# Optimization experiments

Measured on AMD Instinct MI355X. Metric: run time of the kernel, lower is better.

The kernel has to match this reference:

```python
import jax, jax.numpy as jnp
import numpy as np

V, S, D, H, F, L, C = 30522, 1024, 1024, 16, 4096, 3, 5
HD = D // H
EPS = 1e-5


def layer_norm(x, g, b):
    mu = jnp.mean(x, axis=-1, keepdims=True)
    var = jnp.mean((x - mu) ** 2, axis=-1, keepdims=True)
    return (x - mu) * jax.lax.rsqrt(var + EPS) * g + b


def setup_inputs() -> dict:
    key = jax.random.key(0)
    ks = iter(jax.random.split(key, 32))
    s = 0.02
    inp = {
        "input_ids": jax.random.randint(next(ks), (8, S), 0, V),
        "attention_mask": jax.random.randint(next(ks), (8, S), 0, 2),
        "emb": jax.random.normal(next(ks), (V, D), jnp.float32) * s,
        "pos_emb": jax.random.normal(next(ks), (1, S, D), jnp.float32) * s,
        "Wq": jax.random.normal(next(ks), (L, D, D), jnp.float32) * s,
        "bq": jnp.zeros((L, D), jnp.float32),
        "Wk": jax.random.normal(next(ks), (L, D, D), jnp.float32) * s,
        "bk": jnp.zeros((L, D), jnp.float32),
        "Wv": jax.random.normal(next(ks), (L, D, D), jnp.float32) * s,
        "bv": jnp.zeros((L, D), jnp.float32),
        "Wo": jax.random.normal(next(ks), (L, D, D), jnp.float32) * s,
        "bo": jnp.zeros((L, D), jnp.float32),
        "ln1_g": jnp.ones((L, D), jnp.float32),
        "ln1_b": jnp.zeros((L, D), jnp.float32),
        "ln2_g": jnp.ones((L, D), jnp.float32),
        "ln2_b": jnp.zeros((L, D), jnp.float32),
        "W1": jax.random.normal(next(ks), (L, D, F), jnp.float32) * s,
        "b1": jnp.zeros((L, F), jnp.float32),
        "W2": jax.random.normal(next(ks), (L, F, D), jnp.float32) * s,
        "b2": jnp.zeros((L, D), jnp.float32),
        "cls_g": jnp.ones((D,), jnp.float32),
        "cls_b": jnp.zeros((D,), jnp.float32),
        "Wc": jax.random.normal(next(ks), (D, C), jnp.float32) * s,
        "bc": jnp.zeros((C,), jnp.float32),
    }
    return inp


def reference(input_ids, attention_mask, emb, pos_emb, Wq, bq, Wk, bk, Wv, bv,
              Wo, bo, ln1_g, ln1_b, ln2_g, ln2_b, W1, b1, W2, b2,
              cls_g, cls_b, Wc, bc):
    B, Sq = input_ids.shape
    x = emb[input_ids] + pos_emb[:, :Sq, :]  # [B,S,D]
    # mask: [B,1,1,S] broadcast over query positions
    mask = (attention_mask == 0)[:, None, None, :]
    for l in range(L):
        q = (x @ Wq[l] + bq[l]).reshape(B, Sq, H, HD).transpose(0, 2, 1, 3)
        k = (x @ Wk[l] + bk[l]).reshape(B, Sq, H, HD).transpose(0, 2, 1, 3)
        v = (x @ Wv[l] + bv[l]).reshape(B, Sq, H, HD).transpose(0, 2, 1, 3)
        scores = jnp.einsum('bhqd,bhkd->bhqk', q, k) / (HD ** 0.5)
        scores = jnp.where(mask, -1e9, scores)
        attn = jax.nn.softmax(scores, axis=-1)
        ctx = jnp.einsum('bhqk,bhkd->bhqd', attn, v)
        ctx = ctx.transpose(0, 2, 1, 3).reshape(B, Sq, D)
        attn_out = ctx @ Wo[l] + bo[l]
        x = layer_norm(x + attn_out, ln1_g[l], ln1_b[l])
        ff = jax.nn.gelu(x @ W1[l] + b1[l], approximate=False) @ W2[l] + b2[l]
        x = layer_norm(x + ff, ln2_g[l], ln2_b[l])
    cls_tok = x[:, 0, :]
    logits = layer_norm(cls_tok, cls_g, cls_b) @ Wc + bc
    return logits
```

## Files before the change

kernel.cpp:

```cpp
#include <hip/hip_runtime.h>
#include <math.h>

constexpr int S  = 1024;
constexpr int D  = 1024;
constexpr int H  = 16;
constexpr int F  = 4096;
constexpr int NL = 3;
constexpr int C  = 5;
constexpr int HD = 64;
constexpr int B  = 8;
constexpr int MTOK = B * S;

typedef unsigned short u16;
typedef __attribute__((ext_vector_type(4))) float f32x4;
typedef __attribute__((ext_vector_type(4))) int   i32x4;

__device__ inline u16 f2b(float x) {
  unsigned u = __float_as_uint(x);
  unsigned r = (u + 0x7fffu + ((u >> 16) & 1u)) >> 16;
  return (u16)r;
}
__device__ inline float b2f(u16 b) {
  return __uint_as_float(((unsigned)b) << 16);
}

#define GLD16(gptr, lptr)                                                  \
  __builtin_amdgcn_global_load_lds(                                        \
      (const __attribute__((address_space(1))) void*)(gptr),               \
      (__attribute__((address_space(3))) void*)(lptr), 16, 0, 0)

__device__ inline void mfma16(f32x4& acc, i32x4 a, i32x4 b) {
  asm("v_mfma_f32_16x16x32_bf16 %0, %1, %2, %0" : "+v"(acc) : "v"(a), "v"(b));
}

__device__ inline float block_reduce_sum_256(float v, float* red) {
  #pragma unroll
  for (int off = 32; off > 0; off >>= 1) v += __shfl_down(v, off, 64);
  int lane = threadIdx.x & 63, wid = threadIdx.x >> 6;
  if (lane == 0) red[wid] = v;
  __syncthreads();
  float t = red[0] + red[1] + red[2] + red[3];
  __syncthreads();
  return t;
}

__device__ inline float gelu_f(float x) {
  return 0.5f * x * (1.0f + erff(x * 0.70710678118654752f));
}

__global__ __launch_bounds__(256) void embed_kernel(
    const int* __restrict__ ids, const float* __restrict__ emb,
    const float* __restrict__ pos, float* __restrict__ X,
    u16* __restrict__ Xb) {
  int t = blockIdx.x;
  int s = t & (S - 1);
  size_t id = (size_t)ids[t];
  const float4* e = (const float4*)(emb + id * (size_t)D);
  const float4* p = (const float4*)(pos + (size_t)s * D);
  int i = threadIdx.x;
  float4 a = e[i], b = p[i];
  float4 v = make_float4(a.x + b.x, a.y + b.y, a.z + b.z, a.w + b.w);
  ((float4*)(X + (size_t)t * D))[i] = v;
  ushort4 o = {f2b(v.x), f2b(v.y), f2b(v.z), f2b(v.w)};
  *(ushort4*)&Xb[(size_t)t * D + i * 4] = o;
}

__global__ __launch_bounds__(256) void add_ln_kernel(
    const float* __restrict__ X, const float* __restrict__ Y,
    const float* __restrict__ g, const float* __restrict__ bta,
    float* __restrict__ Out, u16* __restrict__ Outb) {
  __shared__ float red[4];
  int t = blockIdx.x, i = threadIdx.x;
  const float4* xr = (const float4*)(X + (size_t)t * D);
  const float4* yr = (const float4*)(Y + (size_t)t * D);
  float4 a = xr[i], b = yr[i];
  float4 v = make_float4(a.x + b.x, a.y + b.y, a.z + b.z, a.w + b.w);
  float sum = v.x + v.y + v.z + v.w;
  sum = block_reduce_sum_256(sum, red);
  float mean = sum * (1.0f / D);
  float dx = v.x - mean, dy = v.y - mean, dz = v.z - mean, dw = v.w - mean;
  float sq = dx * dx + dy * dy + dz * dz + dw * dw;
  sq = block_reduce_sum_256(sq, red);
  float rstd = rsqrtf(sq * (1.0f / D) + 1e-5f);
  float4 gg = ((const float4*)g)[i];
  float4 bb = ((const float4*)bta)[i];
  float4 o = make_float4(dx * rstd * gg.x + bb.x, dy * rstd * gg.y + bb.y,
                         dz * rstd * gg.z + bb.z, dw * rstd * gg.w + bb.w);
  ((float4*)(Out + (size_t)t * D))[i] = o;
  ushort4 ob = {f2b(o.x), f2b(o.y), f2b(o.z), f2b(o.w)};
  *(ushort4*)&Outb[(size_t)t * D + i * 4] = ob;
}

__global__ __launch_bounds__(256) void transpose_cast_kernel(
    const float* __restrict__ W, u16* __restrict__ WT, int K, int N) {
  __shared__ float t[32][33];
  int r = threadIdx.x >> 3, c4 = (threadIdx.x & 7) * 4;
  *(float4*)&t[r][c4] =
      *(const float4*)&W[(size_t)(blockIdx.y * 32 + r) * N + blockIdx.x * 32 + c4];
  __syncthreads();
  int n = blockIdx.x * 32 + r;
  int k = blockIdx.y * 32 + c4;
  ushort4 o = {f2b(t[c4 + 0][r]), f2b(t[c4 + 1][r]),
               f2b(t[c4 + 2][r]), f2b(t[c4 + 3][r])};
  *(ushort4*)&WT[(size_t)n * K + k] = o;
}

template <int MODE>
__global__ __launch_bounds__(256) void gemm_mfma(
    const u16* __restrict__ A, const u16* __restrict__ BT,
    const float* __restrict__ bias, void* __restrict__ Cout,
    int M, int N, int K) {
  __shared__ u16 As[128][32];
  __shared__ u16 Bs[128][32];
  int tid = threadIdx.x;
  int row0 = blockIdx.y * 128, col0 = blockIdx.x * 128;
  int wid = tid >> 6, lane = tid & 63;
  int wr = (wid >> 1) * 64, wc = (wid & 1) * 64;
  int fr = lane & 15, fq = lane >> 4;

  f32x4 acc[4][4];
  #pragma unroll
  for (int m = 0; m < 4; m++)
    #pragma unroll
    for (int n = 0; n < 4; n++) acc[m][n] = (f32x4)(0.0f);

  for (int kt = 0; kt < K; kt += 32) {
    #pragma unroll
    for (int i = 0; i < 2; i++) {
      int f = i * 256 + tid;
      int r = f >> 2, ks = (f & 3) * 8;
      GLD16(A + (size_t)(row0 + r) * K + kt + ks, &As[r][ks]);
    }
    #pragma unroll
    for (int i = 0; i < 2; i++) {
      int f = i * 256 + tid;
      int r = f >> 2, ks = (f & 3) * 8;
      GLD16(BT + (size_t)(col0 + r) * K + kt + ks, &Bs[r][ks]);
    }
    __syncthreads();
    i32x4 av[4], bv[4];
    #pragma unroll
    for (int m = 0; m < 4; m++)
      av[m] = *(const i32x4*)&As[wr + m * 16 + fr][fq * 8];
    #pragma unroll
    for (int n = 0; n < 4; n++)
      bv[n] = *(const i32x4*)&Bs[wc + n * 16 + fr][fq * 8];
    #pragma unroll
    for (int m = 0; m < 4; m++)
      #pragma unroll
      for (int n = 0; n < 4; n++) mfma16(acc[m][n], av[m], bv[n]);
    __syncthreads();
  }

  float* Cf = (float*)Cout;
  u16*   Cb = (u16*)Cout;
  #pragma unroll
  for (int n = 0; n < 4; n++) {
    int c = col0 + wc + n * 16 + fr;
    float bvl = bias[c];
    #pragma unroll
    for (int m = 0; m < 4; m++) {
      int r0 = row0 + wr + m * 16 + fq * 4;
      if (MODE == 3) {
        ushort4 o = {f2b(acc[m][n][0] + bvl), f2b(acc[m][n][1] + bvl),
                     f2b(acc[m][n][2] + bvl), f2b(acc[m][n][3] + bvl)};
        *(ushort4*)&Cb[(size_t)c * MTOK + r0] = o;
      } else {
        #pragma unroll
        for (int j = 0; j < 4; j++) {
          float v = acc[m][n][j] + bvl;
          if (MODE == 2) v = gelu_f(v);
          if (MODE == 0) Cf[(size_t)(r0 + j) * N + c] = v;
          else           Cb[(size_t)(r0 + j) * N + c] = f2b(v);
        }
      }
    }
  }
}

__global__ __launch_bounds__(256) void attn_mfma(
    const u16* __restrict__ Q, const u16* __restrict__ K,
    const u16* __restrict__ Vt, const int* __restrict__ amask,
    u16* __restrict__ CTX) {
  __shared__ u16 Ks[64 * 64];
  __shared__ u16 Vts[64 * 64];
  __shared__ float maskadd[64];
  __shared__ u16 Ps[4][32 * 72];

  int tid = threadIdx.x;
  int wave = tid >> 6, lane = tid & 63;
  int fr = lane & 15, fq = lane >> 4;
  int bh = blockIdx.y, b = bh >> 4, h = bh & 15;
  int q0 = blockIdx.x * 128 + wave * 32;

  i32x4 qa[2][2];
  #pragma unroll
  for (int qf = 0; qf < 2; qf++)
    #pragma unroll
    for (int dblk = 0; dblk < 2; dblk++)
      qa[qf][dblk] = *(const i32x4*)&Q[(size_t)(b * S + q0 + qf * 16 + fr) * D +
                                       h * HD + dblk * 32 + fq * 8];

  f32x4 acc_o[2][4];
  float m_run[2][4], l_run[2][4];
  #pragma unroll
  for (int qf = 0; qf < 2; qf++)
    #pragma unroll
    for (int j = 0; j < 4; j++) {
      m_run[qf][j] = -1e30f;
      l_run[qf][j] = 0.f;
      #pragma unroll
      for (int df = 0; df < 4; df++) acc_o[qf][df][j] = 0.f;
    }

  for (int k0 = 0; k0 < S; k0 += 64) {
    #pragma unroll
    for (int i = 0; i < 2; i++) {
      int fi = i * 256 + tid;
      int r = fi >> 3, sl = fi & 7;
      int src = (sl ^ (r & 7)) * 8;
      GLD16(K + (size_t)(b * S + k0 + r) * D + h * HD + src, &Ks[fi * 8]);
    }
    #pragma unroll
    for (int i = 0; i < 2; i++) {
      int fi = i * 256 + tid;
      int r = fi >> 3, sl = fi & 7;
      int src = (sl ^ (r & 7)) * 8;
      GLD16(Vt + (size_t)(h * HD + r) * MTOK + b * S + k0 + src, &Vts[fi * 8]);
    }
    if (tid < 64) maskadd[tid] = amask[b * S + k0 + tid] ? 0.f : -1e9f;
    __syncthreads();

    float mk[4];
    #pragma unroll
    for (int kkf = 0; kkf < 4; kkf++) mk[kkf] = maskadd[kkf * 16 + fr];

    f32x4 sc[2][4];
    #pragma unroll
    for (int qf = 0; qf < 2; qf++)
      #pragma unroll
      for (int kkf = 0; kkf < 4; kkf++) sc[qf][kkf] = (f32x4)(0.0f);
    #pragma unroll
    for (int kkf = 0; kkf < 4; kkf++) {
      int row = kkf * 16 + fr;
      #pragma unroll
      for (int dblk = 0; dblk < 2; dblk++) {
        i32x4 kb = *(const i32x4*)&Ks[row * 64 + (((dblk * 4 + fq) ^ (row & 7)) * 8)];
        mfma16(sc[0][kkf], qa[0][dblk], kb);
        mfma16(sc[1][kkf], qa[1][dblk], kb);
      }
    }

    #pragma unroll
    for (int qf = 0; qf < 2; qf++) {
      #pragma unroll
      for (int j = 0; j < 4; j++) {
        float s0 = sc[qf][0][j] * 0.125f + mk[0];
        float s1 = sc[qf][1][j] * 0.125f + mk[1];
        float s2 = sc[qf][2][j] * 0.125f + mk[2];
        float s3 = sc[qf][3][j] * 0.125f + mk[3];
        float mx = fmaxf(fmaxf(s0, s1), fmaxf(s2, s3));
        #pragma unroll
        for (int off = 1; off < 16; off <<= 1)
          mx = fmaxf(mx, __shfl_xor(mx, off, 64));
        float mold = m_run[qf][j];
        float mnew = fmaxf(mold, mx);
        float sf = __expf(mold - mnew);
        float p0 = __expf(s0 - mnew), p1 = __expf(s1 - mnew);
        float p2 = __expf(s2 - mnew), p3 = __expf(s3 - mnew);
        float ps = p0 + p1 + p2 + p3;
        #pragma unroll
        for (int off = 1; off < 16; off <<= 1)
          ps += __shfl_xor(ps, off, 64);
        l_run[qf][j] = l_run[qf][j] * sf + ps;
        m_run[qf][j] = mnew;
        #pragma unroll
        for (int df = 0; df < 4; df++) acc_o[qf][df][j] *= sf;
        int prow = (qf * 16 + fq * 4 + j) * 72;
        Ps[wave][prow +  0 + fr] = f2b(p0);
        Ps[wave][prow + 16 + fr] = f2b(p1);
        Ps[wave][prow + 32 + fr] = f2b(p2);
        Ps[wave][prow + 48 + fr] = f2b(p3);
      }
    }

    #pragma unroll
    for (int kkblk = 0; kkblk < 2; kkblk++) {
      i32x4 pa0 = *(const i32x4*)&Ps[wave][(fr) * 72 + kkblk * 32 + fq * 8];
      i32x4 pa1 = *(const i32x4*)&Ps[wave][(16 + fr) * 72 + kkblk * 32 + fq * 8];
      #pragma unroll
      for (int df = 0; df < 4; df++) {
        int row = df * 16 + fr;
        i32x4 vb = *(const i32x4*)&Vts[row * 64 + (((kkblk * 4 + fq) ^ (row & 7)) * 8)];
        mfma16(acc_o[0][df], pa0, vb);
        mfma16(acc_o[1][df], pa1, vb);
      }
    }
    __syncthreads();
  }

  #pragma unroll
  for (int qf = 0; qf < 2; qf++) {
    #pragma unroll
    for (int j = 0; j < 4; j++) {
      float linv = 1.0f / l_run[qf][j];
      size_t base = (size_t)(b * S + q0 + qf * 16 + fq * 4 + j) * D + h * HD;
      #pragma unroll
      for (int df = 0; df < 4; df++)
        CTX[base + df * 16 + fr] = f2b(acc_o[qf][df][j] * linv);
    }
  }
}

__global__ __launch_bounds__(256) void classifier_kernel(
    const float* __restrict__ X, const float* __restrict__ g,
    const float* __restrict__ bta, const float* __restrict__ Wc,
    const float* __restrict__ bc, float* __restrict__ out) {
  __shared__ float red[4];
  __shared__ float xn[D];
  int b = blockIdx.x, i = threadIdx.x;
  const float4* xr = (const float4*)(X + (size_t)b * S * D);
  float4 v = xr[i];
  float sum = v.x + v.y + v.z + v.w;
  sum = block_reduce_sum_256(sum, red);
  float mean = sum * (1.0f / D);
  float dx = v.x - mean, dy = v.y - mean, dz = v.z - mean, dw = v.w - mean;
  float sq = dx * dx + dy * dy + dz * dz + dw * dw;
  sq = block_reduce_sum_256(sq, red);
  float rstd = rsqrtf(sq * (1.0f / D) + 1e-5f);
  float4 gg = ((const float4*)g)[i];
  float4 bb = ((const float4*)bta)[i];
  float4 o = make_float4(dx * rstd * gg.x + bb.x, dy * rstd * gg.y + bb.y,
                         dz * rstd * gg.z + bb.z, dw * rstd * gg.w + bb.w);
  *(float4*)&xn[i * 4] = o;
  __syncthreads();
  for (int c = 0; c < C; c++) {
    float p = 0.f;
    for (int d = i; d < D; d += 256) p += xn[d] * Wc[(size_t)d * C + c];
    p = block_reduce_sum_256(p, red);
    if (i == 0) out[b * C + c] = p + bc[c];
  }
}

extern "C" void kernel_launch(void* const* d_in, const int* in_sizes, int n_in,
                              void* d_out, int out_size, void* d_ws,
                              size_t ws_size, hipStream_t stream) {
  const int*   ids   = (const int*)d_in[0];
  const int*   amask = (const int*)d_in[1];
  const float* emb   = (const float*)d_in[2];
  const float* pos   = (const float*)d_in[3];
  const float* Wq    = (const float*)d_in[4];
  const float* bq    = (const float*)d_in[5];
  const float* Wk    = (const float*)d_in[6];
  const float* bk    = (const float*)d_in[7];
  const float* Wv    = (const float*)d_in[8];
  const float* bv    = (const float*)d_in[9];
  const float* Wo    = (const float*)d_in[10];
  const float* bo    = (const float*)d_in[11];
  const float* ln1g  = (const float*)d_in[12];
  const float* ln1b  = (const float*)d_in[13];
  const float* ln2g  = (const float*)d_in[14];
  const float* ln2b  = (const float*)d_in[15];
  const float* W1    = (const float*)d_in[16];
  const float* b1    = (const float*)d_in[17];
  const float* W2    = (const float*)d_in[18];
  const float* b2    = (const float*)d_in[19];
  const float* cg    = (const float*)d_in[20];
  const float* cb    = (const float*)d_in[21];
  const float* Wc    = (const float*)d_in[22];
  const float* bc    = (const float*)d_in[23];
  float* logits = (float*)d_out;

  const size_t MB = 1u << 20;
  char* w = (char*)d_ws;
  float* X   = (float*)(w + 0 * MB);
  float* Y   = (float*)(w + 32 * MB);
  u16* Xb    = (u16*)(w + 64 * MB);
  u16* Qb    = (u16*)(w + 80 * MB);
  u16* Kbuf  = (u16*)(w + 96 * MB);
  u16* Vt    = (u16*)(w + 112 * MB);
  u16* CTXb  = (u16*)(w + 128 * MB);
  u16* Hh    = (u16*)(w + 80 * MB);
  u16* WTq   = (u16*)(w + 144 * MB);
  u16* WTk   = (u16*)(w + 146 * MB);
  u16* WTv   = (u16*)(w + 148 * MB);
  u16* WTo   = (u16*)(w + 150 * MB);
  u16* WT1   = (u16*)(w + 152 * MB);
  u16* WT2   = (u16*)(w + 160 * MB);

  embed_kernel<<<MTOK, 256, 0, stream>>>(ids, emb, pos, X, Xb);

  dim3 tDD(D / 32, D / 32);
  dim3 tFD(F / 32, D / 32);
  dim3 tDF(D / 32, F / 32);
  dim3 gD(D / 128, MTOK / 128);
  dim3 gF(F / 128, MTOK / 128);

  for (int l = 0; l < NL; l++) {
    transpose_cast_kernel<<<tDD, 256, 0, stream>>>(Wq + (size_t)l * D * D, WTq, D, D);
    transpose_cast_kernel<<<tDD, 256, 0, stream>>>(Wk + (size_t)l * D * D, WTk, D, D);
    transpose_cast_kernel<<<tDD, 256, 0, stream>>>(Wv + (size_t)l * D * D, WTv, D, D);
    transpose_cast_kernel<<<tDD, 256, 0, stream>>>(Wo + (size_t)l * D * D, WTo, D, D);
    transpose_cast_kernel<<<tFD, 256, 0, stream>>>(W1 + (size_t)l * D * F, WT1, D, F);
    transpose_cast_kernel<<<tDF, 256, 0, stream>>>(W2 + (size_t)l * F * D, WT2, F, D);

    gemm_mfma<1><<<gD, 256, 0, stream>>>(Xb, WTq, bq + l * D, Qb,   MTOK, D, D);
    gemm_mfma<1><<<gD, 256, 0, stream>>>(Xb, WTk, bk + l * D, Kbuf, MTOK, D, D);
    gemm_mfma<3><<<gD, 256, 0, stream>>>(Xb, WTv, bv + l * D, Vt,   MTOK, D, D);

    attn_mfma<<<dim3(S / 128, B * H), 256, 0, stream>>>(
        Qb, Kbuf, Vt, amask, CTXb);

    gemm_mfma<0><<<gD, 256, 0, stream>>>(CTXb, WTo, bo + l * D, Y, MTOK, D, D);
    add_ln_kernel<<<MTOK, 256, 0, stream>>>(X, Y, ln1g + l * D, ln1b + l * D, X, Xb);

    gemm_mfma<2><<<gF, 256, 0, stream>>>(Xb, WT1, b1 + l * F, Hh, MTOK, F, D);
    gemm_mfma<0><<<gD, 256, 0, stream>>>(Hh, WT2, b2 + l * D, Y, MTOK, D, F);
    add_ln_kernel<<<MTOK, 256, 0, stream>>>(X, Y, ln2g + l * D, ln2b + l * D, X, Xb);
  }
  classifier_kernel<<<B, 256, 0, stream>>>(X, cg, cb, Wc, bc, logits);
}
```

Measured before the change: 1.721 ms.

## Fuse QKV projections into one GEMM and double-buffer GEMM LDS tiles

The three Q/K/V weight matrices now sit contiguously in the workspace, and the biases are packed per layer, so one GEMM launch with 3*D output columns replaces three launches. A new epilogue mode routes each column segment to Q, K (row-major) or the transposed V buffer. Separately, every GEMM now double-buffers its LDS tiles: the next K-slice is loaded while the current one is computed, and one barrier per iteration is removed. The cost is twice the shared memory per block, which may reduce occupancy.

Result: faster. 1.638 ms (-4.8%).

```diff
diff --git a/kernel.cpp b/kernel.cpp
--- a/kernel.cpp
+++ b/kernel.cpp
@@ -105,13 +105,25 @@
   *(ushort4*)&WT[(size_t)n * K + k] = o;
 }
 
+__global__ __launch_bounds__(256) void pack_bias_kernel(
+    const float* __restrict__ bq, const float* __restrict__ bk,
+    const float* __restrict__ bv, float* __restrict__ Bqkv) {
+  int l = blockIdx.x;
+  for (int i = threadIdx.x; i < 3 * D; i += 256) {
+    int seg = i >> 10, j = i & 1023;
+    const float* src = seg == 0 ? bq : (seg == 1 ? bk : bv);
+    Bqkv[l * 3 * D + i] = src[l * D + j];
+  }
+}
+
 template <int MODE>
 __global__ __launch_bounds__(256) void gemm_mfma(
     const u16* __restrict__ A, const u16* __restrict__ BT,
     const float* __restrict__ bias, void* __restrict__ Cout,
-    int M, int N, int K) {
-  __shared__ u16 As[128][32];
-  __shared__ u16 Bs[128][32];
+    int M, int N, int K,
+    u16* __restrict__ outK, u16* __restrict__ outVt) {
+  __shared__ u16 As[2][128][32];
+  __shared__ u16 Bs[2][128][32];
   int tid = threadIdx.x;
   int row0 = blockIdx.y * 128, col0 = blockIdx.x * 128;
   int wid = tid >> 6, lane = tid & 63;
@@ -124,33 +136,40 @@
     #pragma unroll
     for (int n = 0; n < 4; n++) acc[m][n] = (f32x4)(0.0f);
 
-  for (int kt = 0; kt < K; kt += 32) {
-    #pragma unroll
-    for (int i = 0; i < 2; i++) {
-      int f = i * 256 + tid;
-      int r = f >> 2, ks = (f & 3) * 8;
-      GLD16(A + (size_t)(row0 + r) * K + kt + ks, &As[r][ks]);
-    }
-    #pragma unroll
-    for (int i = 0; i < 2; i++) {
-      int f = i * 256 + tid;
-      int r = f >> 2, ks = (f & 3) * 8;
-      GLD16(BT + (size_t)(col0 + r) * K + kt + ks, &Bs[r][ks]);
-    }
+  int sr = tid >> 2, sks = (tid & 3) * 8;
+  const u16* Abase = A + (size_t)(row0 + sr) * K + sks;
+  const u16* Bbase = BT + (size_t)(col0 + sr) * K + sks;
+
+  auto stage = [&](int bufi, int kt) {
+    GLD16(Abase + kt, &As[bufi][sr][sks]);
+    GLD16(Abase + (size_t)64 * K + kt, &As[bufi][64 + sr][sks]);
+    GLD16(Bbase + kt, &Bs[bufi][sr][sks]);
+    GLD16(Bbase + (size_t)64 * K + kt, &Bs[bufi][64 + sr][sks]);
+  };
+  auto compute = [&](int bufi) {
+    i32x4 av[4], bv[4];
+    #pragma unroll
+    for (int m = 0; m < 4; m++)
+      av[m] = *(const i32x4*)&As[bufi][wr + m * 16 + fr][fq * 8];
+    #pragma unroll
+    for (int n = 0; n < 4; n++)
+      bv[n] = *(const i32x4*)&Bs[bufi][wc + n * 16 + fr][fq * 8];
+    #pragma unroll
+    for (int m = 0; m < 4; m++)
+      #pragma unroll
+      for (int n = 0; n < 4; n++) mfma16(acc[m][n], av[m], bv[n]);
+  };
+
+  stage(0, 0);
+  __syncthreads();
+  int cur = 0;
+  for (int kt = 32; kt < K; kt += 32) {
+    stage(cur ^ 1, kt);
+    compute(cur);
     __syncthreads();
-    i32x4 av[4], bv[4];
-    #pragma unroll
-    for (int m = 0; m < 4; m++)
-      av[m] = *(const i32x4*)&As[wr + m * 16 + fr][fq * 8];
-    #pragma unroll
-    for (int n = 0; n < 4; n++)
-      bv[n] = *(const i32x4*)&Bs[wc + n * 16 + fr][fq * 8];
-    #pragma unroll
-    for (int m = 0; m < 4; m++)
-      #pragma unroll
-      for (int n = 0; n < 4; n++) mfma16(acc[m][n], av[m], bv[n]);
-    __syncthreads();
-  }
+    cur ^= 1;
+  }
+  compute(cur);
 
   float* Cf = (float*)Cout;
   u16*   Cb = (u16*)Cout;
@@ -165,6 +184,18 @@
         ushort4 o = {f2b(acc[m][n][0] + bvl), f2b(acc[m][n][1] + bvl),
                      f2b(acc[m][n][2] + bvl), f2b(acc[m][n][3] + bvl)};
         *(ushort4*)&Cb[(size_t)c * MTOK + r0] = o;
+      } else if (MODE == 4) {
+        int seg = c >> 10, cl = c & 1023;
+        if (seg == 2) {
+          ushort4 o = {f2b(acc[m][n][0] + bvl), f2b(acc[m][n][1] + bvl),
+                       f2b(acc[m][n][2] + bvl), f2b(acc[m][n][3] + bvl)};
+          *(ushort4*)&outVt[(size_t)cl * MTOK + r0] = o;
+        } else {
+          u16* dst = seg == 0 ? Cb : outK;
+          #pragma unroll
+          for (int j = 0; j < 4; j++)
+            dst[(size_t)(r0 + j) * D + cl] = f2b(acc[m][n][j] + bvl);
+        }
       } else {
         #pragma unroll
         for (int j = 0; j < 4; j++) {
@@ -381,19 +412,23 @@
   u16* Vt    = (u16*)(w + 112 * MB);
   u16* CTXb  = (u16*)(w + 128 * MB);
   u16* Hh    = (u16*)(w + 80 * MB);
-  u16* WTq   = (u16*)(w + 144 * MB);
-  u16* WTk   = (u16*)(w + 146 * MB);
-  u16* WTv   = (u16*)(w + 148 * MB);
+  u16* WTqkv = (u16*)(w + 144 * MB);
+  u16* WTq   = WTqkv;
+  u16* WTk   = WTqkv + (size_t)D * D;
+  u16* WTv   = WTqkv + (size_t)2 * D * D;
   u16* WTo   = (u16*)(w + 150 * MB);
   u16* WT1   = (u16*)(w + 152 * MB);
   u16* WT2   = (u16*)(w + 160 * MB);
+  float* Bqkv = (float*)(w + 168 * MB);
 
   embed_kernel<<<MTOK, 256, 0, stream>>>(ids, emb, pos, X, Xb);
+  pack_bias_kernel<<<NL, 256, 0, stream>>>(bq, bk, bv, Bqkv);
 
   dim3 tDD(D / 32, D / 32);
   dim3 tFD(F / 32, D / 32);
   dim3 tDF(D / 32, F / 32);
   dim3 gD(D / 128, MTOK / 128);
+  dim3 gQKV(3 * D / 128, MTOK / 128);
   dim3 gF(F / 128, MTOK / 128);
 
   for (int l = 0; l < NL; l++) {
@@ -404,18 +439,20 @@
     transpose_cast_kernel<<<tFD, 256, 0, stream>>>(W1 + (size_t)l * D * F, WT1, D, F);
     transpose_cast_kernel<<<tDF, 256, 0, stream>>>(W2 + (size_t)l * F * D, WT2, F, D);
 
-    gemm_mfma<1><<<gD, 256, 0, stream>>>(Xb, WTq, bq + l * D, Qb,   MTOK, D, D);
-    gemm_mfma<1><<<gD, 256, 0, stream>>>(Xb, WTk, bk + l * D, Kbuf, MTOK, D, D);
-    gemm_mfma<3><<<gD, 256, 0, stream>>>(Xb, WTv, bv + l * D, Vt,   MTOK, D, D);
+    gemm_mfma<4><<<gQKV, 256, 0, stream>>>(
+        Xb, WTqkv, Bqkv + l * 3 * D, Qb, MTOK, 3 * D, D, Kbuf, Vt);
 
     attn_mfma<<<dim3(S / 128, B * H), 256, 0, stream>>>(
         Qb, Kbuf, Vt, amask, CTXb);
 
-    gemm_mfma<0><<<gD, 256, 0, stream>>>(CTXb, WTo, bo + l * D, Y, MTOK, D, D);
+    gemm_mfma<0><<<gD, 256, 0, stream>>>(CTXb, WTo, bo + l * D, Y, MTOK, D, D,
+                                         nullptr, nullptr);
     add_ln_kernel<<<MTOK, 256, 0, stream>>>(X, Y, ln1g + l * D, ln1b + l * D, X, Xb);
 
-    gemm_mfma<2><<<gF, 256, 0, stream>>>(Xb, WT1, b1 + l * F, Hh, MTOK, F, D);
-    gemm_mfma<0><<<gD, 256, 0, stream>>>(Hh, WT2, b2 + l * D, Y, MTOK, D, F);
+    gemm_mfma<2><<<gF, 256, 0, stream>>>(Xb, WT1, b1 + l * F, Hh, MTOK, F, D,
+                                         nullptr, nullptr);
+    gemm_mfma<0><<<gD, 256, 0, stream>>>(Hh, WT2, b2 + l * D, Y, MTOK, D, F,
+                                         nullptr, nullptr);
     add_ln_kernel<<<MTOK, 256, 0, stream>>>(X, Y, ln2g + l * D, ln2b + l * D, X, Xb);
   }
   classifier_kernel<<<B, 256, 0, stream>>>(X, cg, cb, Wc, bc, logits);
```
